# Optimization experiments

Hardware: AMD Instinct MI355X
Metric: run time of the kernel (lower is better)

The kernel has to match this reference:

```python
import jax, jax.numpy as jnp
import numpy as np

N_NODES = 100000
N_EDGES = 600000
NODE_DIM = 64
EDGE_DIM = 32
HID = 128
OUT = 24


def setup_inputs() -> dict:
    key = jax.random.key(0)
    ks = jax.random.split(key, 20)

    def w(k, shape):
        return jax.random.normal(k, shape, jnp.float32) * (1.0 / np.sqrt(shape[0]).astype(np.float32))

    inp = {}
    inp["x"] = jax.random.normal(ks[0], (N_NODES, NODE_DIM), jnp.float32)
    inp["edge_index"] = jax.random.randint(ks[1], (2, N_EDGES), 0, N_NODES)
    inp["edge_attr"] = jax.random.normal(ks[2], (N_EDGES, EDGE_DIM), jnp.float32)
    inp["lin1_w"] = w(ks[3], (NODE_DIM, HID)); inp["lin1_b"] = jnp.zeros((HID,), jnp.float32)
    i = 4
    for c in (1, 2, 3):
        inp[f"conv{c}_edge_w"] = w(ks[i], (EDGE_DIM, HID)); inp[f"conv{c}_edge_b"] = jnp.zeros((HID,), jnp.float32)
        inp[f"conv{c}_w1"] = w(ks[i + 1], (HID, HID)); inp[f"conv{c}_b1"] = jnp.zeros((HID,), jnp.float32)
        inp[f"conv{c}_w2"] = w(ks[i + 2], (HID, HID)); inp[f"conv{c}_b2"] = jnp.zeros((HID,), jnp.float32)
        i += 3
    inp["cls_w1"] = w(ks[i], (2 * HID + EDGE_DIM, HID)); inp["cls_b1"] = jnp.zeros((HID,), jnp.float32)
    inp["cls_w2"] = w(ks[i + 1], (HID, OUT)); inp["cls_b2"] = jnp.zeros((OUT,), jnp.float32)
    return inp


def _gine(h, src, dst, e_emb, w1, b1, w2, b2, eps=0.0):
    # GINEConv: out = MLP((1+eps)*x + sum_{j->i} relu(x_j + edge_emb))
    m = jax.nn.relu(h[src] + e_emb)                       # [E, HID] gather + fuse
    agg = jax.ops.segment_sum(m, dst, num_segments=N_NODES)  # scatter-add to dst
    z = (1.0 + eps) * h + agg
    return jax.nn.relu(z @ w1 + b1) @ w2 + b2


def reference(x, edge_index, edge_attr,
              lin1_w, lin1_b,
              conv1_edge_w, conv1_edge_b, conv1_w1, conv1_b1, conv1_w2, conv1_b2,
              conv2_edge_w, conv2_edge_b, conv2_w1, conv2_b1, conv2_w2, conv2_b2,
              conv3_edge_w, conv3_edge_b, conv3_w1, conv3_b1, conv3_w2, conv3_b2,
              cls_w1, cls_b1, cls_w2, cls_b2):
    src, dst = edge_index[0], edge_index[1]
    h = x @ lin1_w + lin1_b                               # [N, HID]
    layers = [
        (conv1_edge_w, conv1_edge_b, conv1_w1, conv1_b1, conv1_w2, conv1_b2),
        (conv2_edge_w, conv2_edge_b, conv2_w1, conv2_b1, conv2_w2, conv2_b2),
        (conv3_edge_w, conv3_edge_b, conv3_w1, conv3_b1, conv3_w2, conv3_b2),
    ]
    for ew, eb, w1, b1, w2, b2 in layers:
        e_emb = edge_attr @ ew + eb                       # [E, HID]
        h = jax.nn.relu(_gine(h, src, dst, e_emb, w1, b1, w2, b2))
    edge_feat = jnp.concatenate([h[src], h[dst], edge_attr], axis=-1)  # [E, 2*HID+EDGE_DIM]
    return jax.nn.relu(edge_feat @ cls_w1 + cls_b1) @ cls_w2 + cls_b2  # [E, OUT]
```

## Files before the change

kernel.cpp:

```cpp
#include <hip/hip_runtime.h>

#define N_NODES 100000
#define N_EDGES 600000
#define NODE_DIM 64
#define EDGE_DIM 32
#define HID 128
#define OUT_DIM 24

typedef short short8 __attribute__((ext_vector_type(8)));
typedef short short4v __attribute__((ext_vector_type(4)));
typedef float f32x4 __attribute__((ext_vector_type(4)));

#define MFMA16(a, b, c) __builtin_amdgcn_mfma_f32_16x16x32_bf16(a, b, c, 0, 0, 0)

__device__ inline unsigned short f2bf(float f) {
  unsigned u = __float_as_uint(f);
  u += 0x7FFFu + ((u >> 16) & 1u);
  return (unsigned short)(u >> 16);
}
__device__ inline float bf2f(unsigned short b) {
  return __uint_as_float(((unsigned)b) << 16);
}

#define OFF_CW1T 0
#define OFF_CW2T 36864
#define OFF_LAYER(c) (40960 + (c)*65536)
#define OFF_EWT(c) (237568 + (c)*8192)
#define W_TOTAL 262144

__global__ __launch_bounds__(256) void prep_weights(
    const float* __restrict__ cw1, const float* __restrict__ cw2,
    const float* __restrict__ l0w1, const float* __restrict__ l0w2,
    const float* __restrict__ l1w1, const float* __restrict__ l1w2,
    const float* __restrict__ l2w1, const float* __restrict__ l2w2,
    const float* __restrict__ e0w, const float* __restrict__ e1w,
    const float* __restrict__ e2w,
    unsigned short* __restrict__ wb) {
  int i = blockIdx.x * 256 + threadIdx.x;
  if (i < 36864) {
    int n = i / 288, k = i % 288;
    wb[OFF_CW1T + i] = f2bf(cw1[k * 128 + n]);
  }
  int j = i - 36864;
  if (j >= 0 && j < 4096) {
    int n = j / 128, k = j % 128;
    wb[OFF_CW2T + j] = f2bf(n < 24 ? cw2[k * 24 + n] : 0.f);
  }
  int t = i - 40960;
  if (t >= 0 && t < 3 * 32768) {
    int c = t / 32768, u = t % 32768;
    const float* w = (u < 16384) ? (c == 0 ? l0w1 : c == 1 ? l1w1 : l2w1)
                                 : (c == 0 ? l0w2 : c == 1 ? l1w2 : l2w2);
    int v = u & 16383;
    int n = v >> 7, k = v & 127;
    float val = w[k * 128 + n];
    unsigned short hi = f2bf(val);
    unsigned short lo = f2bf(val - bf2f(hi));
    int base = OFF_LAYER(c) + (u < 16384 ? 0 : 32768);
    wb[base + v] = hi;
    wb[base + 16384 + v] = lo;
  }
  int p = i - 139264;
  if (p >= 0 && p < 3 * 8192) {
    int c = p / 8192, u = p % 8192;
    int v = u & 4095;
    int s = v >> 3, jj = v & 7;
    int ntile = s >> 6, kgrp = (s >> 4) & 3, nrow = s & 15;
    int n = ntile * 16 + nrow, k = kgrp * 8 + jj;
    const float* ew = (c == 0 ? e0w : c == 1 ? e1w : e2w);
    float val = ew[k * 128 + n];
    unsigned short hi = f2bf(val);
    wb[OFF_EWT(c) + u] = (u < 4096) ? hi : f2bf(val - bf2f(hi));
  }
}

__global__ __launch_bounds__(256) void lin1_kernel(
    const float* __restrict__ x, const float* __restrict__ w,
    const float* __restrict__ b, float* __restrict__ h) {
  __shared__ float4 smem4[3072];
  float* sA = (float*)smem4;
  float* sB = (float*)smem4 + 4096;
  int tid = threadIdx.x;
  int tn = tid & 31, tm = tid >> 5;
  int mbase = blockIdx.x * 64;

  for (int i = tid; i < 1024; i += 256) {
    int m = i & 63, k4 = (i >> 6) << 2;
    int row = mbase + m; if (row >= N_NODES) row = N_NODES - 1;
    float4 v = *(const float4*)(x + (size_t)row * NODE_DIM + k4);
    sA[(k4 + 0) * 64 + m] = v.x; sA[(k4 + 1) * 64 + m] = v.y;
    sA[(k4 + 2) * 64 + m] = v.z; sA[(k4 + 3) * 64 + m] = v.w;
  }
  for (int i = tid; i < 2048; i += 256)
    *(float4*)&sB[i * 4] = ((const float4*)w)[i];
  __syncthreads();

  float acc[8][4] = {};
#pragma unroll 8
  for (int k = 0; k < 64; ++k) {
    float4 a0 = *(float4*)&sA[k * 64 + tm * 8];
    float4 a1 = *(float4*)&sA[k * 64 + tm * 8 + 4];
    float4 bv = *(float4*)&sB[k * 128 + tn * 4];
    float av[8] = {a0.x, a0.y, a0.z, a0.w, a1.x, a1.y, a1.z, a1.w};
    float bb[4] = {bv.x, bv.y, bv.z, bv.w};
#pragma unroll
    for (int i = 0; i < 8; ++i)
#pragma unroll
      for (int jj = 0; jj < 4; ++jj) acc[i][jj] = fmaf(av[i], bb[jj], acc[i][jj]);
  }
  float4 bv = *(const float4*)(b + tn * 4);
#pragma unroll
  for (int i = 0; i < 8; ++i) {
    int row = mbase + tm * 8 + i;
    if (row < N_NODES) {
      float4 o = {acc[i][0] + bv.x, acc[i][1] + bv.y, acc[i][2] + bv.z, acc[i][3] + bv.w};
      *(float4*)(h + (size_t)row * HID + tn * 4) = o;
    }
  }
}

__global__ __launch_bounds__(256) void hist_kernel(
    const int* __restrict__ dst, int* __restrict__ counts) {
  int e = blockIdx.x * 256 + threadIdx.x;
  if (e < N_EDGES) atomicAdd(&counts[dst[e]], 1);
}

#define SCAN_BLK 98
__global__ __launch_bounds__(256) void scan_partial(
    const int* __restrict__ cnt, int* __restrict__ partial) {
  __shared__ int sdata[256];
  int b = blockIdx.x, t = threadIdx.x;
  int sum = 0;
  for (int i = t; i < 1024; i += 256) {
    int idx = b * 1024 + i;
    sum += (idx < N_NODES) ? cnt[idx] : 0;
  }
  sdata[t] = sum; __syncthreads();
  for (int s = 128; s > 0; s >>= 1) {
    if (t < s) sdata[t] += sdata[t + s];
    __syncthreads();
  }
  if (t == 0) partial[b] = sdata[0];
}

__global__ void scan_sums(const int* __restrict__ partial,
                          int* __restrict__ partialScan, int* __restrict__ rowptr) {
  if (threadIdx.x == 0) {
    int acc = 0;
    for (int i = 0; i < SCAN_BLK; ++i) { partialScan[i] = acc; acc += partial[i]; }
    rowptr[N_NODES] = acc;
  }
}

__global__ __launch_bounds__(256) void scan_final(
    const int* __restrict__ cnt, const int* __restrict__ partialScan,
    int* __restrict__ rowptr, int* __restrict__ cur) {
  __shared__ int sdata[256];
  int b = blockIdx.x, t = threadIdx.x;
  int i0 = b * 1024 + t * 4;
  int c[4]; int s = 0;
#pragma unroll
  for (int j = 0; j < 4; ++j) {
    c[j] = (i0 + j < N_NODES) ? cnt[i0 + j] : 0;
    s += c[j];
  }
  sdata[t] = s; __syncthreads();
  for (int d = 1; d < 256; d <<= 1) {
    int u = (t >= d) ? sdata[t - d] : 0;
    __syncthreads();
    sdata[t] += u;
    __syncthreads();
  }
  int off = sdata[t] - s + partialScan[b];
#pragma unroll
  for (int j = 0; j < 4; ++j) {
    int idx = i0 + j;
    if (idx < N_NODES) { rowptr[idx] = off; cur[idx] = off; off += c[j]; }
  }
}

__global__ __launch_bounds__(256) void scatter_kernel(
    const int* __restrict__ dst, const int* __restrict__ src,
    int* __restrict__ cur, int* __restrict__ perm, int* __restrict__ srcp) {
  int e = blockIdx.x * 256 + threadIdx.x;
  if (e < N_EDGES) {
    int slot = atomicAdd(&cur[dst[e]], 1);
    perm[slot] = e;
    srcp[slot] = src[e];
  }
}

__global__ __launch_bounds__(256) void build_eafrag(
    const float* __restrict__ ea, const int* __restrict__ perm,
    unsigned short* __restrict__ frag) {
  int slot = blockIdx.x * 256 + threadIdx.x;
  if (slot >= N_EDGES) return;
  int e = perm[slot];
  const float4* row = (const float4*)(ea + (size_t)e * EDGE_DIM);
  unsigned short* dp = frag + ((size_t)(slot >> 7)) * 4096 +
                       (size_t)(((slot & 127) >> 4)) * 512 + (slot & 15) * 8;
#pragma unroll
  for (int kg = 0; kg < 4; ++kg) {
    float4 v0 = row[kg * 2], v1 = row[kg * 2 + 1];
    short8 pk = {(short)f2bf(v0.x), (short)f2bf(v0.y), (short)f2bf(v0.z), (short)f2bf(v0.w),
                 (short)f2bf(v1.x), (short)f2bf(v1.y), (short)f2bf(v1.z), (short)f2bf(v1.w)};
    *(short8*)(dp + kg * 128) = pk;
  }
}

__global__ __launch_bounds__(256) void edge_emb_kernel(
    const float* __restrict__ h, const unsigned short* __restrict__ eafrag,
    const int* __restrict__ srcp, const unsigned short* __restrict__ ewt,
    const float* __restrict__ eb, unsigned short* __restrict__ mout) {
  __shared__ float emb[128 * 132];
  __shared__ int sidx[128];
  int tid = threadIdx.x, lane = tid & 63, wave = tid >> 6;
  int wm = wave & 1, wn = wave >> 1;
  int sbase = blockIdx.x * 128;
  if (tid < 128) {
    int sl = sbase + tid;
    sidx[tid] = (sl < N_EDGES) ? srcp[sl] : 0;
  }
  const short8* Af = (const short8*)(eafrag) + (size_t)blockIdx.x * 512;
  const short8* Bh = (const short8*)(ewt);
  const short8* Bl = (const short8*)(ewt + 4096);
  short8 af[4], bh[4], bl[4];
#pragma unroll
  for (int mt = 0; mt < 4; ++mt) af[mt] = Af[(wm * 4 + mt) * 64 + lane];
#pragma unroll
  for (int nt = 0; nt < 4; ++nt) {
    bh[nt] = Bh[(wn * 4 + nt) * 64 + lane];
    bl[nt] = Bl[(wn * 4 + nt) * 64 + lane];
  }
  const f32x4 zf = {0.f, 0.f, 0.f, 0.f};
  f32x4 acc[4][4];
#pragma unroll
  for (int mt = 0; mt < 4; ++mt)
#pragma unroll
    for (int nt = 0; nt < 4; ++nt) {
      acc[mt][nt] = MFMA16(af[mt], bh[nt], zf);
      acc[mt][nt] = MFMA16(af[mt], bl[nt], acc[mt][nt]);
    }
  int q = lane >> 4, r = lane & 15;
#pragma unroll
  for (int nt = 0; nt < 4; ++nt) {
    int n = wn * 64 + nt * 16 + r;
    float ebv = eb[n];
#pragma unroll
    for (int mt = 0; mt < 4; ++mt) {
      int rowb = (wm * 4 + mt) * 16 + q * 4;
#pragma unroll
      for (int i2 = 0; i2 < 4; ++i2)
        emb[(rowb + i2) * 132 + n] = acc[mt][nt][i2] + ebv;
    }
  }
  __syncthreads();
#pragma unroll
  for (int it = 0; it < 16; ++it) {
    int idx = it * 256 + tid;
    int row = idx >> 5, c4 = (idx & 31) * 4;
    int sl = sbase + row;
    int s = sidx[row];
    float4 hv = *(const float4*)(h + (size_t)s * HID + c4);
    float4 ev = *(const float4*)(emb + row * 132 + c4);
    short4v pk = {(short)f2bf(fmaxf(ev.x + hv.x, 0.f)),
                  (short)f2bf(fmaxf(ev.y + hv.y, 0.f)),
                  (short)f2bf(fmaxf(ev.z + hv.z, 0.f)),
                  (short)f2bf(fmaxf(ev.w + hv.w, 0.f))};
    if (sl < N_EDGES) *(short4v*)(mout + (size_t)sl * HID + c4) = pk;
  }
}

__global__ __launch_bounds__(256) void seg_sum_kernel(
    const unsigned short* __restrict__ m, const int* __restrict__ rowptr,
    float* __restrict__ agg) {
  int lane = threadIdx.x & 63;
  int wid = blockIdx.x * 4 + (threadIdx.x >> 6);
  int nw = gridDim.x * 4;
  const unsigned* mu = (const unsigned*)m;
  for (int node = wid; node < N_NODES; node += nw) {
    int beg = rowptr[node], end = rowptr[node + 1];
    float2 acc = {0.f, 0.f};
    const unsigned* p = mu + (size_t)beg * 64 + lane;
    int n = end - beg;
    int i = 0;
    for (; i + 4 <= n; i += 4) {
      unsigned u0 = p[0], u1 = p[64], u2 = p[128], u3 = p[192];
      p += 256;
      acc.x += __uint_as_float(u0 << 16) + __uint_as_float(u1 << 16) +
               __uint_as_float(u2 << 16) + __uint_as_float(u3 << 16);
      acc.y += __uint_as_float(u0 & 0xffff0000u) + __uint_as_float(u1 & 0xffff0000u) +
               __uint_as_float(u2 & 0xffff0000u) + __uint_as_float(u3 & 0xffff0000u);
    }
    for (; i < n; ++i) {
      unsigned u = p[0];
      p += 64;
      acc.x += __uint_as_float(u << 16);
      acc.y += __uint_as_float(u & 0xffff0000u);
    }
    *(float2*)(agg + (size_t)node * HID + lane * 2) = acc;
  }
}

__global__ __launch_bounds__(256) void agg_gather_kernel(
    const float* __restrict__ h, const float* __restrict__ ea,
    const int* __restrict__ srcp, const int* __restrict__ perm,
    const int* __restrict__ rowptr,
    const float* __restrict__ ew, const float* __restrict__ eb,
    float* __restrict__ agg) {
  int tid = threadIdx.x, lane = tid & 63;
  int wid = blockIdx.x * 4 + (tid >> 6);
  int nwaves = gridDim.x * 4;
  const float2* ew2 = (const float2*)ew;
  float2 ebv = *(const float2*)(eb + lane * 2);

  for (int node = wid; node < N_NODES; node += nwaves) {
    int beg = rowptr[node], end = rowptr[node + 1];
    float2 acc = {0.f, 0.f};
    for (int i = beg; i < end; ++i) {
      int s0 = srcp[i];
      int e0 = perm[i];
      float2 h0 = *(const float2*)(h + (size_t)s0 * HID + lane * 2);
      const float4* ea0 = (const float4*)(ea + (size_t)e0 * EDGE_DIM);
      float2 m0 = ebv;
#pragma unroll
      for (int k4 = 0; k4 < 8; ++k4) {
        float4 a0 = ea0[k4];
        float a0v[4] = {a0.x, a0.y, a0.z, a0.w};
#pragma unroll
        for (int j = 0; j < 4; ++j) {
          float2 w = ew2[(k4 * 4 + j) * 64 + lane];
          m0.x = fmaf(a0v[j], w.x, m0.x);
          m0.y = fmaf(a0v[j], w.y, m0.y);
        }
      }
      acc.x += fmaxf(m0.x + h0.x, 0.f);
      acc.y += fmaxf(m0.y + h0.y, 0.f);
    }
    *(float2*)(agg + (size_t)node * HID + lane * 2) = acc;
  }
}

__global__ __launch_bounds__(256) void mlp_mfma(
    const float* __restrict__ h, const float* __restrict__ agg,
    const unsigned short* __restrict__ wl,
    const float* __restrict__ b1, const float* __restrict__ b2,
    float* __restrict__ hout) {
  __shared__ unsigned short lds[40960];
  unsigned short* sAh = lds;
  unsigned short* sAl = lds + 4096;
  unsigned short* sBh = lds + 8192;
  unsigned short* sBl = lds + 12288;
  unsigned short* t1h = lds;
  unsigned short* t1l = lds + 16384;
  unsigned short* sB2h = lds + 32768;
  unsigned short* sB2l = lds + 36864;
  const unsigned short* w1h = wl;
  const unsigned short* w1l = wl + 16384;
  const unsigned short* w2h = wl + 32768;
  const unsigned short* w2l = wl + 49152;
  int tid = threadIdx.x, lane = tid & 63, wave = tid >> 6;
  int wm = wave & 1, wn = wave >> 1;
  int mbase = blockIdx.x * 128;
  const f32x4 zf = {0.f, 0.f, 0.f, 0.f};

  f32x4 acc[4][4];
#pragma unroll
  for (int a = 0; a < 4; ++a)
#pragma unroll
    for (int bq = 0; bq < 4; ++bq) acc[a][bq] = zf;

  for (int c = 0; c < 4; ++c) {
    __syncthreads();
#pragma unroll
    for (int it = 0; it < 4; ++it) {
      int idx = it * 256 + tid;
      int m = idx >> 3, k4 = (idx & 7) * 4;
      int row = mbase + m; if (row >= N_NODES) row = N_NODES - 1;
      size_t g = (size_t)row * HID + c * 32 + k4;
      float4 hv = *(const float4*)(h + g);
      float4 av = *(const float4*)(agg + g);
      float z0 = hv.x + av.x, z1 = hv.y + av.y, z2 = hv.z + av.z, z3 = hv.w + av.w;
      unsigned short h0 = f2bf(z0), h1 = f2bf(z1), h2 = f2bf(z2), h3 = f2bf(z3);
      int slot = ((m >> 4) * 4 + (k4 >> 3)) * 16 + (m & 15);
      int off = slot * 8 + (k4 & 7);
      short4v ph = {(short)h0, (short)h1, (short)h2, (short)h3};
      short4v pl = {(short)f2bf(z0 - bf2f(h0)), (short)f2bf(z1 - bf2f(h1)),
                    (short)f2bf(z2 - bf2f(h2)), (short)f2bf(z3 - bf2f(h3))};
      *(short4v*)(sAh + off) = ph;
      *(short4v*)(sAl + off) = pl;
    }
#pragma unroll
    for (int it = 0; it < 2; ++it) {
      int s = it * 256 + tid;
      int ntile = s >> 6, kgrp = (s >> 4) & 3, nrow = s & 15;
      int goff = (ntile * 16 + nrow) * 128 + c * 32 + kgrp * 8;
      *(short8*)(sBh + s * 8) = *(const short8*)(w1h + goff);
      *(short8*)(sBl + s * 8) = *(const short8*)(w1l + goff);
    }
    __syncthreads();
    short8 ah[4], al[4], bh[4], bl[4];
#pragma unroll
    for (int mt = 0; mt < 4; ++mt) {
      ah[mt] = *(short8*)(sAh + ((wm * 4 + mt) * 64 + lane) * 8);
      al[mt] = *(short8*)(sAl + ((wm * 4 + mt) * 64 + lane) * 8);
    }
#pragma unroll
    for (int nt = 0; nt < 4; ++nt) {
      bh[nt] = *(short8*)(sBh + ((wn * 4 + nt) * 64 + lane) * 8);
      bl[nt] = *(short8*)(sBl + ((wn * 4 + nt) * 64 + lane) * 8);
    }
#pragma unroll
    for (int mt = 0; mt < 4; ++mt)
#pragma unroll
      for (int nt = 0; nt < 4; ++nt) {
        acc[mt][nt] = MFMA16(ah[mt], bh[nt], acc[mt][nt]);
        acc[mt][nt] = MFMA16(ah[mt], bl[nt], acc[mt][nt]);
        acc[mt][nt] = MFMA16(al[mt], bh[nt], acc[mt][nt]);
      }
  }
  __syncthreads();
  int q = lane >> 4, r = lane & 15;
#pragma unroll
  for (int nt = 0; nt < 4; ++nt) {
    int n = wn * 64 + nt * 16 + r;
    float b1v = b1[n];
    int kgrp = n >> 3, jj = n & 7;
#pragma unroll
    for (int mt = 0; mt < 4; ++mt) {
      int mtg = wm * 4 + mt;
#pragma unroll
      for (int i2 = 0; i2 < 4; ++i2) {
        int mrow = q * 4 + i2;
        float val = fmaxf(acc[mt][nt][i2] + b1v, 0.f);
        unsigned short hi = f2bf(val);
        int idx = ((mtg * 16 + kgrp) * 16 + mrow) * 8 + jj;
        t1h[idx] = hi;
        t1l[idx] = f2bf(val - bf2f(hi));
      }
    }
  }

  f32x4 acc2[4][4];
#pragma unroll
  for (int a = 0; a < 4; ++a)
#pragma unroll
    for (int bq = 0; bq < 4; ++bq) acc2[a][bq] = zf;

  for (int kc = 0; kc < 4; ++kc) {
    __syncthreads();
#pragma unroll
    for (int it = 0; it < 2; ++it) {
      int s = it * 256 + tid;
      int ntile = s >> 6, kgrp = (s >> 4) & 3, nrow = s & 15;
      int goff = (ntile * 16 + nrow) * 128 + kc * 32 + kgrp * 8;
      *(short8*)(sB2h + s * 8) = *(const short8*)(w2h + goff);
      *(short8*)(sB2l + s * 8) = *(const short8*)(w2l + goff);
    }
    __syncthreads();
    short8 ah[4], al[4], bh[4], bl[4];
#pragma unroll
    for (int mt = 0; mt < 4; ++mt) {
      int mtg = wm * 4 + mt;
      int idx = ((mtg * 16 + kc * 4 + q) * 16 + r) * 8;
      ah[mt] = *(short8*)(t1h + idx);
      al[mt] = *(short8*)(t1l + idx);
    }
#pragma unroll
    for (int nt = 0; nt < 4; ++nt) {
      bh[nt] = *(short8*)(sB2h + ((wn * 4 + nt) * 64 + lane) * 8);
      bl[nt] = *(short8*)(sB2l + ((wn * 4 + nt) * 64 + lane) * 8);
    }
#pragma unroll
    for (int mt = 0; mt < 4; ++mt)
#pragma unroll
      for (int nt = 0; nt < 4; ++nt) {
        acc2[mt][nt] = MFMA16(ah[mt], bh[nt], acc2[mt][nt]);
        acc2[mt][nt] = MFMA16(ah[mt], bl[nt], acc2[mt][nt]);
        acc2[mt][nt] = MFMA16(al[mt], bh[nt], acc2[mt][nt]);
      }
  }
#pragma unroll
  for (int nt = 0; nt < 4; ++nt) {
    int n = wn * 64 + nt * 16 + r;
    float b2v = b2[n];
#pragma unroll
    for (int mt = 0; mt < 4; ++mt) {
      int mtg = wm * 4 + mt;
#pragma unroll
      for (int i2 = 0; i2 < 4; ++i2) {
        int row = mbase + mtg * 16 + q * 4 + i2;
        if (row < N_NODES)
          hout[(size_t)row * HID + n] = fmaxf(acc2[mt][nt][i2] + b2v, 0.f);
      }
    }
  }
}

__global__ __launch_bounds__(256) void cls_mfma(
    const float* __restrict__ h, const float* __restrict__ ea,
    const int* __restrict__ src, const int* __restrict__ dst,
    const unsigned short* __restrict__ w1t, const unsigned short* __restrict__ w2t,
    const float* __restrict__ b1, const float* __restrict__ b2,
    float* __restrict__ out) {
  __shared__ unsigned short lds[20480];
  unsigned short* sA = lds;
  unsigned short* sB = lds + 4096;
  unsigned short* t1 = lds;
  unsigned short* sB2 = lds + 16384;
  __shared__ int sidx[256];
  int tid = threadIdx.x, lane = tid & 63, wave = tid >> 6;
  int wm = wave & 1, wn = wave >> 1;
  int ebase = blockIdx.x * 128;
  const f32x4 zf = {0.f, 0.f, 0.f, 0.f};

  {
    int e0 = ebase + (tid & 127);
    if (e0 >= N_EDGES) e0 = N_EDGES - 1;
    sidx[tid] = (tid < 128 ? src : dst)[e0];
  }

  f32x4 acc[4][4];
#pragma unroll
  for (int a = 0; a < 4; ++a)
#pragma unroll
    for (int bq = 0; bq < 4; ++bq) acc[a][bq] = zf;

  for (int c = 0; c < 9; ++c) {
    __syncthreads();
#pragma unroll
    for (int it = 0; it < 4; ++it) {
      int idx = it * 256 + tid;
      int m = idx >> 3, k4 = (idx & 7) * 4;
      const float* rp;
      if (c < 4)      rp = h + (size_t)sidx[m] * HID + c * 32 + k4;
      else if (c < 8) rp = h + (size_t)sidx[128 + m] * HID + (c - 4) * 32 + k4;
      else {
        int e8 = ebase + m; if (e8 >= N_EDGES) e8 = N_EDGES - 1;
        rp = ea + (size_t)e8 * EDGE_DIM + k4;
      }
      float4 v = *(const float4*)rp;
      int slot = ((m >> 4) * 4 + (k4 >> 3)) * 16 + (m & 15);
      short4v pk = {(short)f2bf(v.x), (short)f2bf(v.y), (short)f2bf(v.z), (short)f2bf(v.w)};
      *(short4v*)(sA + slot * 8 + (k4 & 7)) = pk;
    }
#pragma unroll
    for (int it = 0; it < 2; ++it) {
      int s = it * 256 + tid;
      int ntile = s >> 6, kgrp = (s >> 4) & 3, nrow = s & 15;
      *(short8*)(sB + s * 8) = *(const short8*)(w1t + (ntile * 16 + nrow) * 288 + c * 32 + kgrp * 8);
    }
    __syncthreads();
    short8 af[4], bfv[4];
#pragma unroll
    for (int mt = 0; mt < 4; ++mt)
      af[mt] = *(short8*)(sA + ((wm * 4 + mt) * 64 + lane) * 8);
#pragma unroll
    for (int nt = 0; nt < 4; ++nt)
      bfv[nt] = *(short8*)(sB + ((wn * 4 + nt) * 64 + lane) * 8);
#pragma unroll
    for (int mt = 0; mt < 4; ++mt)
#pragma unroll
      for (int nt = 0; nt < 4; ++nt)
        acc[mt][nt] = MFMA16(af[mt], bfv[nt], acc[mt][nt]);
  }
  __syncthreads();
  int q = lane >> 4, r = lane & 15;
#pragma unroll
  for (int nt = 0; nt < 4; ++nt) {
    int n = wn * 64 + nt * 16 + r;
    float b1v = b1[n];
    int kgrp = n >> 3, jj = n & 7;
#pragma unroll
    for (int mt = 0; mt < 4; ++mt) {
      int mtg = wm * 4 + mt;
#pragma unroll
      for (int i2 = 0; i2 < 4; ++i2) {
        int mrow = q * 4 + i2;
        float val = fmaxf(acc[mt][nt][i2] + b1v, 0.f);
        t1[((mtg * 16 + kgrp) * 16 + mrow) * 8 + jj] = f2bf(val);
      }
    }
  }
#pragma unroll
  for (int it = 0; it < 2; ++it) {
    int s = it * 256 + tid;
    int ntile = s >> 8, kgrp = (s >> 4) & 15, nrow = s & 15;
    *(short8*)(sB2 + s * 8) = *(const short8*)(w2t + (ntile * 16 + nrow) * 128 + kgrp * 8);
  }
  __syncthreads();

  f32x4 acc2[2][2];
  acc2[0][0] = zf; acc2[0][1] = zf; acc2[1][0] = zf; acc2[1][1] = zf;
#pragma unroll
  for (int kc = 0; kc < 4; ++kc) {
    short8 a0 = *(short8*)(t1 + (((wave * 2 + 0) * 16 + kc * 4 + q) * 16 + r) * 8);
    short8 a1 = *(short8*)(t1 + (((wave * 2 + 1) * 16 + kc * 4 + q) * 16 + r) * 8);
    short8 b0 = *(short8*)(sB2 + ((0 * 16 + kc * 4 + q) * 16 + r) * 8);
    short8 b1f = *(short8*)(sB2 + ((1 * 16 + kc * 4 + q) * 16 + r) * 8);
    acc2[0][0] = MFMA16(a0, b0, acc2[0][0]);
    acc2[0][1] = MFMA16(a0, b1f, acc2[0][1]);
    acc2[1][0] = MFMA16(a1, b0, acc2[1][0]);
    acc2[1][1] = MFMA16(a1, b1f, acc2[1][1]);
  }
#pragma unroll
  for (int nt2 = 0; nt2 < 2; ++nt2) {
    int n = nt2 * 16 + r;
    float b2v = (n < OUT_DIM) ? b2[n] : 0.f;
#pragma unroll
    for (int mt2 = 0; mt2 < 2; ++mt2) {
      int mtg = wave * 2 + mt2;
#pragma unroll
      for (int i2 = 0; i2 < 4; ++i2) {
        int e = ebase + mtg * 16 + q * 4 + i2;
        if (n < OUT_DIM && e < N_EDGES)
          out[(size_t)e * OUT_DIM + n] = acc2[mt2][nt2][i2] + b2v;
      }
    }
  }
}

extern "C" void kernel_launch(void* const* d_in, const int* in_sizes, int n_in,
                              void* d_out, int out_size, void* d_ws, size_t ws_size,
                              hipStream_t stream) {
  const float* x = (const float*)d_in[0];
  const int* ei = (const int*)d_in[1];
  const float* ea = (const float*)d_in[2];
  const float* lin1_w = (const float*)d_in[3];
  const float* lin1_b = (const float*)d_in[4];
  const int* src = ei;
  const int* dst = ei + N_EDGES;

  const size_t NH = (size_t)N_NODES * HID;
  float* bufA = (float*)d_ws;
  float* bufB = bufA + NH;
  int* ibase = (int*)(bufB + NH);
  int* rowptr = ibase;
  int* cur = ibase + 100004;
  int* counts = ibase + 200004;
  int* perm = ibase + 300004;
  int* partial = ibase + 900004;
  int* partialScan = ibase + 900132;
  int* srcp = ibase + 900260;
  unsigned short* mbuf = (unsigned short*)(ibase + 1500264);
  unsigned short* eafrag = mbuf + (size_t)N_EDGES * HID;
  size_t need = (size_t)((char*)(eafrag + (size_t)N_EDGES * EDGE_DIM) - (char*)d_ws) +
                (size_t)W_TOTAL * 2 + 4096;
  bool big = ws_size >= need;
  unsigned short* wbase = (unsigned short*)((((uintptr_t)d_ws + ws_size) - (size_t)W_TOTAL * 2) & ~(uintptr_t)255);

  prep_weights<<<(163840 + 255) / 256, 256, 0, stream>>>(
      (const float*)d_in[23], (const float*)d_in[25],
      (const float*)d_in[7], (const float*)d_in[9],
      (const float*)d_in[13], (const float*)d_in[15],
      (const float*)d_in[19], (const float*)d_in[21],
      (const float*)d_in[5], (const float*)d_in[11], (const float*)d_in[17],
      wbase);

  lin1_kernel<<<(N_NODES + 63) / 64, 256, 0, stream>>>(x, lin1_w, lin1_b, bufA);

  hipMemsetAsync(counts, 0, N_NODES * sizeof(int), stream);
  hist_kernel<<<(N_EDGES + 255) / 256, 256, 0, stream>>>(dst, counts);
  scan_partial<<<SCAN_BLK, 256, 0, stream>>>(counts, partial);
  scan_sums<<<1, 64, 0, stream>>>(partial, partialScan, rowptr);
  scan_final<<<SCAN_BLK, 256, 0, stream>>>(counts, partialScan, rowptr, cur);
  scatter_kernel<<<(N_EDGES + 255) / 256, 256, 0, stream>>>(dst, src, cur, perm, srcp);
  if (big)
    build_eafrag<<<(N_EDGES + 255) / 256, 256, 0, stream>>>(ea, perm, eafrag);

  float* hcur = bufA;
  float* aux = bufB;
  for (int c = 0; c < 3; ++c) {
    const float* ew = (const float*)d_in[5 + c * 6 + 0];
    const float* eb = (const float*)d_in[5 + c * 6 + 1];
    const float* b1 = (const float*)d_in[5 + c * 6 + 3];
    const float* b2 = (const float*)d_in[5 + c * 6 + 5];
    if (big) {
      edge_emb_kernel<<<(N_EDGES + 127) / 128, 256, 0, stream>>>(
          hcur, eafrag, srcp, wbase + OFF_EWT(c), eb, mbuf);
      seg_sum_kernel<<<2048, 256, 0, stream>>>(mbuf, rowptr, aux);
    } else {
      agg_gather_kernel<<<2048, 256, 0, stream>>>(
          hcur, ea, srcp, perm, rowptr, ew, eb, aux);
    }
    mlp_mfma<<<(N_NODES + 127) / 128, 256, 0, stream>>>(
        hcur, aux, wbase + OFF_LAYER(c), b1, b2, aux);
    float* tmp = hcur; hcur = aux; aux = tmp;
  }

  const float* cb1 = (const float*)d_in[24];
  const float* cb2 = (const float*)d_in[26];
  cls_mfma<<<(N_EDGES + 127) / 128, 256, 0, stream>>>(
      hcur, ea, src, dst, wbase + OFF_CW1T, wbase + OFF_CW2T, cb1, cb2, (float*)d_out);
}
```

Before: 1.018 ms.

## Fuse edge embedding with segmented scatter-add and keep bf16 node features

Merges the edge-embedding and segment-sum kernels into one. Each block sums runs of consecutive edges that share a destination (edges are sorted by dst) and writes them to agg, plain-storing runs that lie fully inside the block and using atomics only at the boundaries. This removes the bf16 message buffer write and read of size E x 128. Node features are also written as a bf16 copy so the gathers in the edge and classifier kernels move half the bytes. The cost is an extra memset of agg per layer, atomics at block boundaries, and a float accumulation order that is no longer deterministic.

```diff
diff --git a/kernel.cpp b/kernel.cpp
--- a/kernel.cpp
+++ b/kernel.cpp
@@ -76,7 +76,8 @@
 
 __global__ __launch_bounds__(256) void lin1_kernel(
     const float* __restrict__ x, const float* __restrict__ w,
-    const float* __restrict__ b, float* __restrict__ h) {
+    const float* __restrict__ b, float* __restrict__ h,
+    unsigned short* __restrict__ hbf) {
   __shared__ float4 smem4[3072];
   float* sA = (float*)smem4;
   float* sB = (float*)smem4 + 4096;
@@ -115,6 +116,8 @@
     if (row < N_NODES) {
       float4 o = {acc[i][0] + bv.x, acc[i][1] + bv.y, acc[i][2] + bv.z, acc[i][3] + bv.w};
       *(float4*)(h + (size_t)row * HID + tn * 4) = o;
+      short4v pk = {(short)f2bf(o.x), (short)f2bf(o.y), (short)f2bf(o.z), (short)f2bf(o.w)};
+      *(short4v*)(hbf + (size_t)row * HID + tn * 4) = pk;
     }
   }
 }
@@ -181,12 +184,15 @@
 
 __global__ __launch_bounds__(256) void scatter_kernel(
     const int* __restrict__ dst, const int* __restrict__ src,
-    int* __restrict__ cur, int* __restrict__ perm, int* __restrict__ srcp) {
+    int* __restrict__ cur, int* __restrict__ perm,
+    int* __restrict__ srcp, int* __restrict__ dstp) {
   int e = blockIdx.x * 256 + threadIdx.x;
   if (e < N_EDGES) {
-    int slot = atomicAdd(&cur[dst[e]], 1);
+    int d = dst[e];
+    int slot = atomicAdd(&cur[d], 1);
     perm[slot] = e;
     srcp[slot] = src[e];
+    dstp[slot] = d;
   }
 }
 
@@ -208,18 +214,22 @@
   }
 }
 
-__global__ __launch_bounds__(256) void edge_emb_kernel(
-    const float* __restrict__ h, const unsigned short* __restrict__ eafrag,
-    const int* __restrict__ srcp, const unsigned short* __restrict__ ewt,
-    const float* __restrict__ eb, unsigned short* __restrict__ mout) {
+__global__ __launch_bounds__(256) void edge_agg_kernel(
+    const unsigned short* __restrict__ hbf, const unsigned short* __restrict__ eafrag,
+    const int* __restrict__ srcp, const int* __restrict__ dstp,
+    const unsigned short* __restrict__ ewt, const float* __restrict__ eb,
+    float* __restrict__ agg) {
   __shared__ float emb[128 * 132];
   __shared__ int sidx[128];
+  __shared__ int sdst[128];
   int tid = threadIdx.x, lane = tid & 63, wave = tid >> 6;
   int wm = wave & 1, wn = wave >> 1;
   int sbase = blockIdx.x * 128;
+  int nrows = N_EDGES - sbase; if (nrows > 128) nrows = 128;
   if (tid < 128) {
     int sl = sbase + tid;
     sidx[tid] = (sl < N_EDGES) ? srcp[sl] : 0;
+    sdst[tid] = (sl < N_EDGES) ? dstp[sl] : -1;
   }
   const short8* Af = (const short8*)(eafrag) + (size_t)blockIdx.x * 512;
   const short8* Bh = (const short8*)(ewt);
@@ -255,50 +265,40 @@
     }
   }
   __syncthreads();
-#pragma unroll
-  for (int it = 0; it < 16; ++it) {
-    int idx = it * 256 + tid;
-    int row = idx >> 5, c4 = (idx & 31) * 4;
-    int sl = sbase + row;
-    int s = sidx[row];
-    float4 hv = *(const float4*)(h + (size_t)s * HID + c4);
-    float4 ev = *(const float4*)(emb + row * 132 + c4);
-    short4v pk = {(short)f2bf(fmaxf(ev.x + hv.x, 0.f)),
-                  (short)f2bf(fmaxf(ev.y + hv.y, 0.f)),
-                  (short)f2bf(fmaxf(ev.z + hv.z, 0.f)),
-                  (short)f2bf(fmaxf(ev.w + hv.w, 0.f))};
-    if (sl < N_EDGES) *(short4v*)(mout + (size_t)sl * HID + c4) = pk;
-  }
-}
-
-__global__ __launch_bounds__(256) void seg_sum_kernel(
-    const unsigned short* __restrict__ m, const int* __restrict__ rowptr,
-    float* __restrict__ agg) {
-  int lane = threadIdx.x & 63;
-  int wid = blockIdx.x * 4 + (threadIdx.x >> 6);
-  int nw = gridDim.x * 4;
-  const unsigned* mu = (const unsigned*)m;
-  for (int node = wid; node < N_NODES; node += nw) {
-    int beg = rowptr[node], end = rowptr[node + 1];
-    float2 acc = {0.f, 0.f};
-    const unsigned* p = mu + (size_t)beg * 64 + lane;
-    int n = end - beg;
-    int i = 0;
-    for (; i + 4 <= n; i += 4) {
-      unsigned u0 = p[0], u1 = p[64], u2 = p[128], u3 = p[192];
-      p += 256;
-      acc.x += __uint_as_float(u0 << 16) + __uint_as_float(u1 << 16) +
-               __uint_as_float(u2 << 16) + __uint_as_float(u3 << 16);
-      acc.y += __uint_as_float(u0 & 0xffff0000u) + __uint_as_float(u1 & 0xffff0000u) +
-               __uint_as_float(u2 & 0xffff0000u) + __uint_as_float(u3 & 0xffff0000u);
-    }
-    for (; i < n; ++i) {
-      unsigned u = p[0];
-      p += 64;
-      acc.x += __uint_as_float(u << 16);
-      acc.y += __uint_as_float(u & 0xffff0000u);
-    }
-    *(float2*)(agg + (size_t)node * HID + lane * 2) = acc;
+  {
+    int r0 = wave * 32;
+#pragma unroll 4
+    for (int rr = 0; rr < 32; ++rr) {
+      int row = r0 + rr;
+      int s = sidx[row];
+      unsigned u = *(const unsigned*)(hbf + (size_t)s * HID + lane * 2);
+      float2 ev = *(float2*)(emb + row * 132 + lane * 2);
+      ev.x = fmaxf(ev.x + bf2f((unsigned short)u), 0.f);
+      ev.y = fmaxf(ev.y + bf2f((unsigned short)(u >> 16)), 0.f);
+      *(float2*)(emb + row * 132 + lane * 2) = ev;
+    }
+  }
+  __syncthreads();
+  {
+    int hh = tid >> 7;
+    int col = tid & 127;
+    int rbeg = hh * 64;
+    int rend = rbeg + 64; if (rend > nrows) rend = nrows;
+    if (rbeg < rend) {
+      float a = 0.f;
+      int cnode = sdst[rbeg];
+      bool atomic_first = true;
+      for (int rr = rbeg; rr < rend; ++rr) {
+        int node = sdst[rr];
+        if (node != cnode) {
+          if (atomic_first) atomicAdd(&agg[(size_t)cnode * HID + col], a);
+          else agg[(size_t)cnode * HID + col] = a;
+          a = 0.f; cnode = node; atomic_first = false;
+        }
+        a += emb[rr * 132 + col];
+      }
+      atomicAdd(&agg[(size_t)cnode * HID + col], a);
+    }
   }
 }
 
@@ -345,7 +345,7 @@
     const float* __restrict__ h, const float* __restrict__ agg,
     const unsigned short* __restrict__ wl,
     const float* __restrict__ b1, const float* __restrict__ b2,
-    float* __restrict__ hout) {
+    float* __restrict__ hout, unsigned short* __restrict__ hbfout) {
   __shared__ unsigned short lds[40960];
   unsigned short* sAh = lds;
   unsigned short* sAl = lds + 4096;
@@ -490,15 +490,18 @@
 #pragma unroll
       for (int i2 = 0; i2 < 4; ++i2) {
         int row = mbase + mtg * 16 + q * 4 + i2;
-        if (row < N_NODES)
-          hout[(size_t)row * HID + n] = fmaxf(acc2[mt][nt][i2] + b2v, 0.f);
+        if (row < N_NODES) {
+          float val = fmaxf(acc2[mt][nt][i2] + b2v, 0.f);
+          hout[(size_t)row * HID + n] = val;
+          hbfout[(size_t)row * HID + n] = f2bf(val);
+        }
       }
     }
   }
 }
 
 __global__ __launch_bounds__(256) void cls_mfma(
-    const float* __restrict__ h, const float* __restrict__ ea,
+    const unsigned short* __restrict__ hbf, const float* __restrict__ ea,
     const int* __restrict__ src, const int* __restrict__ dst,
     const unsigned short* __restrict__ w1t, const unsigned short* __restrict__ w2t,
     const float* __restrict__ b1, const float* __restrict__ b2,
@@ -528,21 +531,27 @@
 
   for (int c = 0; c < 9; ++c) {
     __syncthreads();
-#pragma unroll
-    for (int it = 0; it < 4; ++it) {
-      int idx = it * 256 + tid;
-      int m = idx >> 3, k4 = (idx & 7) * 4;
-      const float* rp;
-      if (c < 4)      rp = h + (size_t)sidx[m] * HID + c * 32 + k4;
-      else if (c < 8) rp = h + (size_t)sidx[128 + m] * HID + (c - 4) * 32 + k4;
-      else {
+    if (c < 8) {
+#pragma unroll
+      for (int it = 0; it < 2; ++it) {
+        int idx = it * 256 + tid;
+        int kgrp = idx >> 7, m = idx & 127;
+        int node = (c < 4) ? sidx[m] : sidx[128 + m];
+        int cc = (c & 3) * 32;
+        short8 v = *(const short8*)(hbf + (size_t)node * HID + cc + kgrp * 8);
+        *(short8*)(sA + (((m >> 4) * 4 + kgrp) * 16 + (m & 15)) * 8) = v;
+      }
+    } else {
+#pragma unroll
+      for (int it = 0; it < 4; ++it) {
+        int idx = it * 256 + tid;
+        int m = idx >> 3, k4 = (idx & 7) * 4;
         int e8 = ebase + m; if (e8 >= N_EDGES) e8 = N_EDGES - 1;
-        rp = ea + (size_t)e8 * EDGE_DIM + k4;
-      }
-      float4 v = *(const float4*)rp;
-      int slot = ((m >> 4) * 4 + (k4 >> 3)) * 16 + (m & 15);
-      short4v pk = {(short)f2bf(v.x), (short)f2bf(v.y), (short)f2bf(v.z), (short)f2bf(v.w)};
-      *(short4v*)(sA + slot * 8 + (k4 & 7)) = pk;
+        float4 v = *(const float4*)(ea + (size_t)e8 * EDGE_DIM + k4);
+        int slot = ((m >> 4) * 4 + (k4 >> 3)) * 16 + (m & 15);
+        short4v pk = {(short)f2bf(v.x), (short)f2bf(v.y), (short)f2bf(v.z), (short)f2bf(v.w)};
+        *(short4v*)(sA + slot * 8 + (k4 & 7)) = pk;
+      }
     }
 #pragma unroll
     for (int it = 0; it < 2; ++it) {
@@ -642,8 +651,9 @@
   int* partial = ibase + 900004;
   int* partialScan = ibase + 900132;
   int* srcp = ibase + 900260;
-  unsigned short* mbuf = (unsigned short*)(ibase + 1500264);
-  unsigned short* eafrag = mbuf + (size_t)N_EDGES * HID;
+  int* dstp = ibase + 1500260;
+  unsigned short* hbf = (unsigned short*)(ibase + 2100264);
+  unsigned short* eafrag = hbf + (size_t)N_NODES * HID;
   size_t need = (size_t)((char*)(eafrag + (size_t)N_EDGES * EDGE_DIM) - (char*)d_ws) +
                 (size_t)W_TOTAL * 2 + 4096;
   bool big = ws_size >= need;
@@ -657,14 +667,14 @@
       (const float*)d_in[5], (const float*)d_in[11], (const float*)d_in[17],
       wbase);
 
-  lin1_kernel<<<(N_NODES + 63) / 64, 256, 0, stream>>>(x, lin1_w, lin1_b, bufA);
+  lin1_kernel<<<(N_NODES + 63) / 64, 256, 0, stream>>>(x, lin1_w, lin1_b, bufA, hbf);
 
   hipMemsetAsync(counts, 0, N_NODES * sizeof(int), stream);
   hist_kernel<<<(N_EDGES + 255) / 256, 256, 0, stream>>>(dst, counts);
   scan_partial<<<SCAN_BLK, 256, 0, stream>>>(counts, partial);
   scan_sums<<<1, 64, 0, stream>>>(partial, partialScan, rowptr);
   scan_final<<<SCAN_BLK, 256, 0, stream>>>(counts, partialScan, rowptr, cur);
-  scatter_kernel<<<(N_EDGES + 255) / 256, 256, 0, stream>>>(dst, src, cur, perm, srcp);
+  scatter_kernel<<<(N_EDGES + 255) / 256, 256, 0, stream>>>(dst, src, cur, perm, srcp, dstp);
   if (big)
     build_eafrag<<<(N_EDGES + 255) / 256, 256, 0, stream>>>(ea, perm, eafrag);
 
@@ -676,20 +686,20 @@
     const float* b1 = (const float*)d_in[5 + c * 6 + 3];
     const float* b2 = (const float*)d_in[5 + c * 6 + 5];
     if (big) {
-      edge_emb_kernel<<<(N_EDGES + 127) / 128, 256, 0, stream>>>(
-          hcur, eafrag, srcp, wbase + OFF_EWT(c), eb, mbuf);
-      seg_sum_kernel<<<2048, 256, 0, stream>>>(mbuf, rowptr, aux);
+      hipMemsetAsync(aux, 0, NH * sizeof(float), stream);
+      edge_agg_kernel<<<(N_EDGES + 127) / 128, 256, 0, stream>>>(
+          hbf, eafrag, srcp, dstp, wbase + OFF_EWT(c), eb, aux);
     } else {
       agg_gather_kernel<<<2048, 256, 0, stream>>>(
           hcur, ea, srcp, perm, rowptr, ew, eb, aux);
     }
     mlp_mfma<<<(N_NODES + 127) / 128, 256, 0, stream>>>(
-        hcur, aux, wbase + OFF_LAYER(c), b1, b2, aux);
+        hcur, aux, wbase + OFF_LAYER(c), b1, b2, aux, hbf);
     float* tmp = hcur; hcur = aux; aux = tmp;
   }
 
   const float* cb1 = (const float*)d_in[24];
   const float* cb2 = (const float*)d_in[26];
   cls_mfma<<<(N_EDGES + 127) / 128, 256, 0, stream>>>(
-      hcur, ea, src, dst, wbase + OFF_CW1T, wbase + OFF_CW2T, cb1, cb2, (float*)d_out);
-}
+      hbf, ea, src, dst, wbase + OFF_CW1T, wbase + OFF_CW2T, cb1, cb2, (float*)d_out);
+}
```

New measurement: 1.024 ms. No clear change (+0.6%).
